# Kernel tuning notes

Measured on AMD Instinct MI355X. Metric: run time of the kernel, lower is better.

## Reference

```python
import jax, jax.numpy as jnp
import numpy as np

D_MODEL = 256
N_LAYERS = 4
D_STATE = 16
EXPAND = 2
D_CONV = 4
D_INNER = EXPAND * D_MODEL
DT_RANK = (D_MODEL + 15) // 16  # ceil(d_model/16) = 16
BATCH = 8
SEQ = 2048
EPS = 1e-5


def setup_inputs() -> dict:
    key = jax.random.key(0)
    ks = jax.random.split(key, 12)
    rn = lambda k, s, sc=0.02: jax.random.normal(k, s, dtype=jnp.float32) * sc
    A_log = jnp.log(jnp.broadcast_to(jnp.arange(1, D_STATE + 1, dtype=jnp.float32),
                                     (N_LAYERS, D_INNER, D_STATE)))
    return {
        "x": jax.random.normal(ks[0], (BATCH, SEQ, 2), dtype=jnp.float32),
        "w_in": rn(ks[1], (D_MODEL, 2), 0.5),
        "b_in": jnp.zeros((D_MODEL,), jnp.float32),
        "norm_w": jnp.ones((N_LAYERS, D_MODEL), jnp.float32),
        "in_proj_w": rn(ks[2], (N_LAYERS, 2 * D_INNER, D_MODEL)),
        "conv_w": rn(ks[3], (N_LAYERS, D_INNER, 1, D_CONV), 0.1),
        "conv_b": jnp.zeros((N_LAYERS, D_INNER), jnp.float32),
        "x_proj_w": rn(ks[4], (N_LAYERS, DT_RANK + 2 * D_STATE, D_INNER)),
        "dt_proj_w": rn(ks[5], (N_LAYERS, D_INNER, DT_RANK), 0.1),
        "dt_proj_b": rn(ks[6], (N_LAYERS, D_INNER), 0.1),
        "A_log": A_log,
        "D_skip": jnp.ones((N_LAYERS, D_INNER), jnp.float32),
        "out_proj_w": rn(ks[7], (N_LAYERS, D_MODEL, D_INNER)),
        "w_head": rn(ks[8], (1, D_MODEL), 0.1),
        "b_head": jnp.zeros((1,), jnp.float32),
    }


def _rmsnorm(x, w):
    return x * jax.lax.rsqrt(jnp.mean(x * x, axis=-1, keepdims=True) + EPS) * w


def _causal_dw_conv(x, w, b):
    # x: (B, L, C); w: (C, 1, K) depthwise; causal left-pad K-1
    xt = jnp.swapaxes(x, 1, 2)  # (B, C, L)
    y = jax.lax.conv_general_dilated(xt, w, (1,), [(D_CONV - 1, 0)],
                                     dimension_numbers=("NCH", "OIH", "NCH"),
                                     feature_group_count=D_INNER)
    return jnp.swapaxes(y + b[None, :, None], 1, 2)


def _selective_scan(u, delta, A, Bm, Cm, Dp):
    # u, delta: (B, L, E); A: (E, N); Bm, Cm: (B, L, N); Dp: (E,)
    dA = jnp.exp(delta[..., None] * A)                 # (B, L, E, N)
    dBu = (delta * u)[..., None] * Bm[:, :, None, :]   # (B, L, E, N)

    def step(h, t):
        dA_t, dBu_t = t
        h = dA_t * h + dBu_t
        return h, h

    h0 = jnp.zeros((u.shape[0], A.shape[0], A.shape[1]), u.dtype)
    _, hs = jax.lax.scan(step, h0, (jnp.swapaxes(dA, 0, 1), jnp.swapaxes(dBu, 0, 1)))
    y = jnp.einsum("lben,bln->ble", hs, Cm)            # (B, L, E)
    return y + u * Dp


def _mamba_block(x, in_w, cw, cb, xp_w, dtw, dtb, A_log, Dp, out_w):
    xz = x @ in_w.T                                    # (B, L, 2E)
    u, z = jnp.split(xz, 2, axis=-1)
    u = jax.nn.silu(_causal_dw_conv(u, cw, cb))
    dbc = u @ xp_w.T                                   # (B, L, dt_rank + 2N)
    delta = jax.nn.softplus(dbc[..., :DT_RANK] @ dtw.T + dtb)
    Bm = dbc[..., DT_RANK:DT_RANK + D_STATE]
    Cm = dbc[..., DT_RANK + D_STATE:]
    y = _selective_scan(u, delta, -jnp.exp(A_log), Bm, Cm, Dp)
    return (y * jax.nn.silu(z)) @ out_w.T


def reference(x, w_in, b_in, norm_w, in_proj_w, conv_w, conv_b, x_proj_w,
              dt_proj_w, dt_proj_b, A_log, D_skip, out_proj_w, w_head, b_head):
    h = x @ w_in.T + b_in                              # (B, L, d_model)
    for i in range(N_LAYERS):
        h = h + _mamba_block(_rmsnorm(h, norm_w[i]), in_proj_w[i], conv_w[i],
                             conv_b[i], x_proj_w[i], dt_proj_w[i], dt_proj_b[i],
                             A_log[i], D_skip[i], out_proj_w[i])
    return (h @ w_head.T + b_head)[..., 0]             # (B, L)
```

## Files before the change

kernel.cpp:

```cpp
#include <hip/hip_runtime.h>
#include <hip/hip_bf16.h>

#define BATCH 8
#define SEQ   2048
#define DM    256
#define DI    512
#define DS    16
#define DTR   16
#define NL    4
#define ROWS  (BATCH*SEQ)
#define NCH   32
#define CHL   64
#define NF    576

typedef __attribute__((ext_vector_type(8))) __bf16 bh8;
typedef __attribute__((ext_vector_type(4))) float f4;

#if __has_builtin(__builtin_amdgcn_exp2f)
#define EXP2(x) __builtin_amdgcn_exp2f(x)
#else
#define EXP2(x) exp2f(x)
#endif
#define LOG2E 1.4426950408889634f

__device__ __forceinline__ float bf2f(unsigned short u) {
    union { unsigned int i; float f; } v; v.i = ((unsigned int)u) << 16; return v.f;
}
__device__ __forceinline__ float4 us4f(ushort4 q) {
    return make_float4(bf2f(q.x), bf2f(q.y), bf2f(q.z), bf2f(q.w));
}
__device__ __forceinline__ float ldg1(const void* p, int i, int bf) {
    if (bf) return bf2f(((const unsigned short*)p)[i]);
    return ((const float*)p)[i];
}
__device__ __forceinline__ float4 ldg4(const void* p, int i, int bf) {
    if (bf) return us4f(*(const ushort4*)(((const unsigned short*)p) + i));
    return *(const float4*)(((const float*)p) + i);
}
__device__ __forceinline__ unsigned short f2bs(float f) {
    union { float f; unsigned u; } x; x.f = f;
    unsigned r = (x.u + 0x7fffu + ((x.u >> 16) & 1u)) >> 16;
    return (unsigned short)r;
}
__device__ __forceinline__ float fsilu(float x) {
    return x * __builtin_amdgcn_rcpf(1.0f + __expf(-x));
}
__device__ __forceinline__ float fsoftplus(float x) {
    return (x > 15.0f) ? x : __logf(1.0f + __expf(x));
}
__device__ __forceinline__ void pow16(float e1, float* pw) {
    float p2 = e1 * e1, p3 = p2 * e1, p4 = p2 * p2;
    float p5 = p4 * e1, p6 = p4 * p2, p7 = p4 * p3, p8 = p4 * p4;
    pw[0] = e1; pw[1] = p2; pw[2] = p3; pw[3] = p4;
    pw[4] = p5; pw[5] = p6; pw[6] = p7; pw[7] = p8;
    pw[8]  = p8 * e1; pw[9]  = p8 * p2; pw[10] = p8 * p3; pw[11] = p8 * p4;
    pw[12] = p8 * p5; pw[13] = p8 * p6; pw[14] = p8 * p7; pw[15] = p8 * p8;
}

typedef const __attribute__((address_space(1))) unsigned int* gas_t;
typedef __attribute__((address_space(3))) unsigned int* las_t;
__device__ __forceinline__ void gl16(const void* g, void* l) {
    __builtin_amdgcn_global_load_lds((gas_t)g, (las_t)l, 16, 0, 0);
}

__global__ void k_probe(const void* x, const void* A_log, int* flag) {
    int t = threadIdx.x;
    float v = bf2f(((const unsigned short*)x)[2 * t]);
    int bad = (fabsf(v) < 32.0f) ? 0 : 1;
    for (int o = 1; o < 64; o <<= 1) bad += __shfl_xor(bad, o);
    int bf = (bad > 8) ? 0 : 1;
    int nb = 0;
    for (int j = 0; j < 64; j++) {
        int e = ((j * 64 + t) * 17) & 32767;
        int n = e & 15;
        float a = ldg1(A_log, e, bf);
        float ea = __expf(a);
        if (fabsf(ea - (float)(n + 1)) > 0.02f * (float)(n + 1)) nb = 1;
    }
    for (int o = 1; o < 64; o <<= 1) nb += __shfl_xor(nb, o);
    if (t == 0) { flag[0] = bf; flag[1] = (nb == 0) ? 1 : 0; }
}

__global__ __launch_bounds__(256) void k_prep(const void* dtw, const void* xpw,
                                              unsigned short* Wc, const int* flag) {
    int bf = *flag;
    int blk = blockIdx.x;
    int l = blk / NF, r = blk % NF;
    int t = threadIdx.x;
    unsigned short* out = Wc + ((size_t)l * NF + r) * DI;
#pragma unroll
    for (int p = 0; p < 2; p++) {
        int k = t + p * 256;
        float v = 0.0f;
        if (r < 512) {
            const int db = l * DI * DTR + r * DTR;
            const int xb = l * 48 * DI;
#pragma unroll
            for (int j = 0; j < 16; j++)
                v = fmaf(ldg1(dtw, db + j, bf), ldg1(xpw, xb + j * DI + k, bf), v);
        } else if (r < 544) {
            v = ldg1(xpw, l * 48 * DI + (16 + r - 512) * DI + k, bf);
        }
        out[k] = f2bs(v);
    }
}

__global__ __launch_bounds__(256) void k_prepw(const void* ipw, const void* norm_w,
                                               unsigned short* Wip, const int* flag) {
    int bf = *flag;
    int blk = blockIdx.x;
    int l = blk >> 10, r = blk & 1023;
    int t = threadIdx.x;
    float v = ldg1(ipw, (l * 1024 + r) * 256 + t, bf) * ldg1(norm_w, l * 256 + t, bf);
    Wip[((size_t)l * 1024 + r) * 256 + t] = f2bs(v);
}

__global__ __launch_bounds__(256) void k_inproj(const void* x, const void* w_in, const void* b_in,
                                                unsigned short* h, float* rssq, const int* flag) {
    int bf = *flag;
    int row = blockIdx.x, e = threadIdx.x;
    float x0 = ldg1(x, row * 2 + 0, bf), x1 = ldg1(x, row * 2 + 1, bf);
    float w0 = ldg1(w_in, e * 2 + 0, bf), w1 = ldg1(w_in, e * 2 + 1, bf);
    float bb = ldg1(b_in, e, bf);
    unsigned short hb = f2bs(fmaf(x0, w0, fmaf(x1, w1, bb)));
    h[(size_t)row * DM + e] = hb;
    float hv = bf2f(hb);
    float ss = hv * hv;
#pragma unroll
    for (int o = 1; o < 64; o <<= 1) ss += __shfl_xor(ss, o);
    if ((e & 63) == 0) rssq[(size_t)row * 4 + (e >> 6)] = ss;
}

#define ASTR 72

__global__ __launch_bounds__(256, 4) void k_ipconv(const unsigned short* A, const unsigned short* W,
                                                   int w_off, unsigned short* xz, unsigned short* u,
                                                   const float* rssq, const void* cw, const void* cb,
                                                   int layer, const int* flag) {
    int bf = *flag;
    constexpr int K = DM;
    constexpr int TSTR = 136;
    __shared__ unsigned short SMEM[144 * TSTR];
    unsigned short* As  = SMEM;
    unsigned short* As2 = SMEM + 8192;
    unsigned short* Ws  = SMEM + 9216;

    int bm = blockIdx.x, bn = blockIdx.y;
    bool ublk = (bn < 4);
    int t = threadIdx.x;
    int w = t >> 6, lane = t & 63;
    int wm = w >> 1, wn = w & 1;
    int lr = lane & 15, quad = lane >> 4;
    int crow = lane >> 3;
    int ccol = ((lane & 7) ^ (lane >> 3)) * 8;

    f4 acc[4][4];
    f4 acc5[4];
#pragma unroll
    for (int i = 0; i < 4; i++) {
        acc5[i] = f4{0.f, 0.f, 0.f, 0.f};
#pragma unroll
        for (int j = 0; j < 4; j++) acc[i][j] = f4{0.f, 0.f, 0.f, 0.f};
    }

    for (int k0 = 0; k0 < K; k0 += 64) {
        __syncthreads();
#pragma unroll
        for (int i = 0; i < 4; i++) {
            int ci = w * 4 + i;
            int r = ci * 8 + crow;
            gl16(A + (size_t)(bm * 128 + r) * K + k0 + ccol, &As[ci * 512]);
        }
        if (ublk && w < 2) {
            int rg = bm * 128 - 16 + w * 8 + crow;
            if (rg < 0) rg = 0;
            gl16(A + (size_t)rg * K + k0 + ccol, &As2[w * 512]);
        }
#pragma unroll
        for (int i = 0; i < 4; i++) {
            int ci = w * 4 + i;
            int r = ci * 8 + crow;
            gl16(W + (size_t)w_off + (size_t)(bn * 128 + r) * K + k0 + ccol, &Ws[ci * 512]);
        }
        __syncthreads();
#pragma unroll
        for (int ks = 0; ks < 64; ks += 32) {
            int csw = (ks + quad * 8) ^ ((lr & 7) << 3);
            bh8 af[4];
#pragma unroll
            for (int i = 0; i < 4; i++)
                af[i] = *(const bh8*)&As[(wm * 64 + i * 16 + lr) * 64 + csw];
            bh8 wf[4];
#pragma unroll
            for (int j = 0; j < 4; j++)
                wf[j] = *(const bh8*)&Ws[(wn * 64 + j * 16 + lr) * 64 + csw];
#pragma unroll
            for (int i = 0; i < 4; i++)
#pragma unroll
                for (int j = 0; j < 4; j++)
                    acc[i][j] = __builtin_amdgcn_mfma_f32_16x16x32_bf16(af[i], wf[j], acc[i][j], 0, 0, 0);
            if (ublk && wm == 0) {
                bh8 a5 = *(const bh8*)&As2[lr * 64 + csw];
#pragma unroll
                for (int j = 0; j < 4; j++)
                    acc5[j] = __builtin_amdgcn_mfma_f32_16x16x32_bf16(a5, wf[j], acc5[j], 0, 0, 0);
            }
        }
    }
    __syncthreads();
    unsigned short* Tile = SMEM;
#pragma unroll
    for (int i = 0; i < 4; i++) {
        int rl = wm * 64 + i * 16 + quad * 4;
        float sc4[4];
#pragma unroll
        for (int r = 0; r < 4; r++) {
            float4 q4 = *(const float4*)&rssq[(size_t)(bm * 128 + rl + r) * 4];
            sc4[r] = rsqrtf((q4.x + q4.y + q4.z + q4.w) * (1.0f / (float)DM) + 1e-5f);
        }
#pragma unroll
        for (int j = 0; j < 4; j++) {
            int cl = wn * 64 + j * 16 + lr;
#pragma unroll
            for (int r = 0; r < 4; r++)
                Tile[(rl + r) * TSTR + cl] = f2bs(acc[i][j][r] * sc4[r]);
        }
    }
    if (ublk && wm == 0) {
#pragma unroll
        for (int r = 0; r < 4; r++) {
            int er = quad * 4 + r;
            int rg = bm * 128 - 16 + er;
            if (rg < 0) rg = 0;
            float4 q4 = *(const float4*)&rssq[(size_t)rg * 4];
            float sc = rsqrtf((q4.x + q4.y + q4.z + q4.w) * (1.0f / (float)DM) + 1e-5f);
#pragma unroll
            for (int j = 0; j < 4; j++) {
                int cl = wn * 64 + j * 16 + lr;
                Tile[(128 + er) * TSTR + cl] = f2bs(acc5[j][r] * sc);
            }
        }
    }
    __syncthreads();
    if (!ublk) {
#pragma unroll
        for (int i = 0; i < 8; i++) {
            int ch = t + i * 256;
            int r = ch >> 4, qc = (ch & 15) * 8;
            uint4 v = *(uint4*)&Tile[r * TSTR + qc];
            *(uint4*)&xz[(size_t)(bm * 128 + r) * 1024 + bn * 128 + qc] = v;
        }
    } else {
        int col4 = t & 31, rowg = t >> 5;
        int c0 = col4 * 4;
        int dg = bn * 128 + c0;
        float4 wv0 = ldg4(cw, (layer * DI + dg + 0) * 4, bf);
        float4 wv1 = ldg4(cw, (layer * DI + dg + 1) * 4, bf);
        float4 wv2 = ldg4(cw, (layer * DI + dg + 2) * 4, bf);
        float4 wv3 = ldg4(cw, (layer * DI + dg + 3) * 4, bf);
        float4 bb = ldg4(cb, layer * DI + dg, bf);
        bool bstart = ((bm & 15) == 0);
        int r0 = rowg * 16;
        auto ldrow = [&](int q) -> float4 {
            if (q < 0) {
                if (bstart) return make_float4(0.f, 0.f, 0.f, 0.f);
                return us4f(*(const ushort4*)&Tile[(144 + q) * TSTR + c0]);
            }
            return us4f(*(const ushort4*)&Tile[q * TSTR + c0]);
        };
        float4 xm3 = ldrow(r0 - 3), xm2 = ldrow(r0 - 2), xm1 = ldrow(r0 - 1);
        for (int rr = r0; rr < r0 + 16; rr++) {
            float4 x0 = us4f(*(const ushort4*)&Tile[rr * TSTR + c0]);
            float a0 = bb.x; a0 = fmaf(wv0.x, xm3.x, a0); a0 = fmaf(wv0.y, xm2.x, a0); a0 = fmaf(wv0.z, xm1.x, a0); a0 = fmaf(wv0.w, x0.x, a0);
            float a1 = bb.y; a1 = fmaf(wv1.x, xm3.y, a1); a1 = fmaf(wv1.y, xm2.y, a1); a1 = fmaf(wv1.z, xm1.y, a1); a1 = fmaf(wv1.w, x0.y, a1);
            float a2 = bb.z; a2 = fmaf(wv2.x, xm3.z, a2); a2 = fmaf(wv2.y, xm2.z, a2); a2 = fmaf(wv2.z, xm1.z, a2); a2 = fmaf(wv2.w, x0.z, a2);
            float a3 = bb.w; a3 = fmaf(wv3.x, xm3.w, a3); a3 = fmaf(wv3.y, xm2.w, a3); a3 = fmaf(wv3.z, xm1.w, a3); a3 = fmaf(wv3.w, x0.w, a3);
            ushort4 o = { f2bs(fsilu(a0)), f2bs(fsilu(a1)), f2bs(fsilu(a2)), f2bs(fsilu(a3)) };
            *(ushort4*)&u[(size_t)(bm * 128 + rr) * DI + dg] = o;
            xm3 = xm2; xm2 = xm1; xm1 = x0;
        }
    }
}

template <int BN, bool ADD, bool SCALE, bool RSUM, bool WINT>
__global__ __launch_bounds__(256, 4) void k_mfma(const unsigned short* A, const void* W, int w_off,
                                                 unsigned short* Cp, float* rssq,
                                                 int N, int K, const int* flag) {
    int bf = *flag;
    __shared__ unsigned short SMEM[(128 + BN) * ASTR];
    unsigned short* As = SMEM;
    unsigned short* Ws = SMEM + 128 * 64;
    constexpr int NT = BN / 32;
    constexpr int TSTR = BN + 8;

    int bm = blockIdx.x, bn = blockIdx.y;
    int t = threadIdx.x;
    int w = t >> 6, lane = t & 63;
    int wm = w >> 1, wn = w & 1;
    int lr = lane & 15, quad = lane >> 4;
    int crow = lane >> 3;
    int ccol = ((lane & 7) ^ (lane >> 3)) * 8;

    f4 acc[4][NT];
#pragma unroll
    for (int i = 0; i < 4; i++)
#pragma unroll
        for (int j = 0; j < NT; j++) acc[i][j] = f4{0.f, 0.f, 0.f, 0.f};

    for (int k0 = 0; k0 < K; k0 += 64) {
        __syncthreads();
#pragma unroll
        for (int i = 0; i < 4; i++) {
            int ci = w * 4 + i;
            int r = ci * 8 + crow;
            gl16(A + (size_t)(bm * 128 + r) * K + k0 + ccol, &As[ci * 512]);
        }
        if (WINT || bf) {
#pragma unroll
            for (int i = 0; i < BN / 32; i++) {
                int ci = w * (BN / 32) + i;
                int r = ci * 8 + crow;
                gl16((const unsigned short*)W + (size_t)w_off +
                         (size_t)(bn * BN + r) * K + k0 + ccol,
                     &Ws[ci * 512]);
            }
        } else {
#pragma unroll
            for (int i = 0; i < BN * 8 / 256; i++) {
                int ch = t + i * 256;
                int r = ch >> 3, kc = (ch & 7) * 8;
                size_t off = (size_t)w_off + (size_t)(bn * BN + r) * K + k0 + kc;
                const float* src = (const float*)W + off;
                float4 a0 = *(const float4*)src;
                float4 a1 = *(const float4*)(src + 4);
                ushort4 v0 = { f2bs(a0.x), f2bs(a0.y), f2bs(a0.z), f2bs(a0.w) };
                ushort4 v1 = { f2bs(a1.x), f2bs(a1.y), f2bs(a1.z), f2bs(a1.w) };
                unsigned short* dst = &Ws[r * 64 + (kc ^ ((r & 7) << 3))];
                *(ushort4*)dst = v0;
                *(ushort4*)(dst + 4) = v1;
            }
        }
        __syncthreads();
#pragma unroll
        for (int ks = 0; ks < 64; ks += 32) {
            int csw = (ks + quad * 8) ^ ((lr & 7) << 3);
            bh8 af[4];
#pragma unroll
            for (int i = 0; i < 4; i++)
                af[i] = *(const bh8*)&As[(wm * 64 + i * 16 + lr) * 64 + csw];
            bh8 wf[NT];
#pragma unroll
            for (int j = 0; j < NT; j++)
                wf[j] = *(const bh8*)&Ws[(wn * (BN / 2) + j * 16 + lr) * 64 + csw];
#pragma unroll
            for (int i = 0; i < 4; i++)
#pragma unroll
                for (int j = 0; j < NT; j++)
                    acc[i][j] = __builtin_amdgcn_mfma_f32_16x16x32_bf16(af[i], wf[j], acc[i][j], 0, 0, 0);
        }
    }
    __syncthreads();
    unsigned short* Tile = SMEM;
#pragma unroll
    for (int i = 0; i < 4; i++) {
        int rl = wm * 64 + i * 16 + quad * 4;
        float sc4[4];
        if (SCALE) {
#pragma unroll
            for (int r = 0; r < 4; r++) {
                float4 q4 = *(const float4*)&rssq[(size_t)(bm * 128 + rl + r) * 4];
                sc4[r] = rsqrtf((q4.x + q4.y + q4.z + q4.w) * (1.0f / (float)DM) + 1e-5f);
            }
        }
#pragma unroll
        for (int j = 0; j < NT; j++) {
            int cl = wn * (BN / 2) + j * 16 + lr;
#pragma unroll
            for (int r = 0; r < 4; r++) {
                float vv = acc[i][j][r];
                if (SCALE) vv *= sc4[r];
                Tile[(rl + r) * TSTR + cl] = f2bs(vv);
            }
        }
    }
    __syncthreads();
    constexpr int CPT = 128 * BN / 8 / 256;
#pragma unroll
    for (int i = 0; i < CPT; i++) {
        int ch = t + i * 256;
        int r = ch / (BN / 8), qc = (ch % (BN / 8)) * 8;
        uint4 v = *(uint4*)&Tile[r * TSTR + qc];
        size_t gidx = (size_t)(bm * 128 + r) * N + bn * BN + qc;
        if (ADD) {
            uint4 c = *(uint4*)&Cp[gidx];
            unsigned short* vp = (unsigned short*)&v;
            unsigned short* cp2 = (unsigned short*)&c;
            uint4 ov;
            unsigned short* op = (unsigned short*)&ov;
            float ssq = 0.0f;
#pragma unroll
            for (int e = 0; e < 8; e++) {
                op[e] = f2bs(bf2f(vp[e]) + bf2f(cp2[e]));
                if (RSUM) { float hv = bf2f(op[e]); ssq = fmaf(hv, hv, ssq); }
            }
            *(uint4*)&Cp[gidx] = ov;
            if (RSUM) {
#pragma unroll
                for (int o2 = 1; o2 < 8; o2 <<= 1) ssq += __shfl_xor(ssq, o2);
                if ((lane & 7) == 0) rssq[(size_t)(bm * 128 + r) * 4 + bn] = ssq;
            }
        } else {
            *(uint4*)&Cp[gidx] = v;
        }
    }
}

__global__ __launch_bounds__(256, 4) void k_fused(const unsigned short* A, const unsigned short* Wc,
                                                  int w_off, unsigned short* delta, float* BC,
                                                  const void* dtb, int layer, const int* flag) {
    int bf = *flag;
    __shared__ unsigned short SMEM[(128 + 64) * ASTR];
    unsigned short* As = SMEM;
    unsigned short* Ws = SMEM + 128 * 64;
    constexpr int TSTR = 72;

    int bm = blockIdx.x, bn = blockIdx.y;
    int t = threadIdx.x;
    int w = t >> 6, lane = t & 63;
    int wm = w >> 1, wn = w & 1;
    int lr = lane & 15, quad = lane >> 4;
    int crow = lane >> 3;
    int ccol = ((lane & 7) ^ (lane >> 3)) * 8;

    f4 acc[4][2];
#pragma unroll
    for (int i = 0; i < 4; i++)
#pragma unroll
        for (int j = 0; j < 2; j++) acc[i][j] = f4{0.f, 0.f, 0.f, 0.f};

    for (int k0 = 0; k0 < DI; k0 += 64) {
        __syncthreads();
#pragma unroll
        for (int i = 0; i < 4; i++) {
            int ci = w * 4 + i;
            int r = ci * 8 + crow;
            gl16(A + (size_t)(bm * 128 + r) * DI + k0 + ccol, &As[ci * 512]);
        }
#pragma unroll
        for (int i = 0; i < 2; i++) {
            int ci = w * 2 + i;
            int r = ci * 8 + crow;
            gl16(Wc + (size_t)w_off + (size_t)(bn * 64 + r) * DI + k0 + ccol, &Ws[ci * 512]);
        }
        __syncthreads();
#pragma unroll
        for (int ks = 0; ks < 64; ks += 32) {
            int csw = (ks + quad * 8) ^ ((lr & 7) << 3);
            bh8 af[4];
#pragma unroll
            for (int i = 0; i < 4; i++)
                af[i] = *(const bh8*)&As[(wm * 64 + i * 16 + lr) * 64 + csw];
            bh8 wf[2];
#pragma unroll
            for (int j = 0; j < 2; j++)
                wf[j] = *(const bh8*)&Ws[(wn * 32 + j * 16 + lr) * 64 + csw];
#pragma unroll
            for (int i = 0; i < 4; i++)
#pragma unroll
                for (int j = 0; j < 2; j++)
                    acc[i][j] = __builtin_amdgcn_mfma_f32_16x16x32_bf16(af[i], wf[j], acc[i][j], 0, 0, 0);
        }
    }
    if (bn < 8) {
        __syncthreads();
        unsigned short* Tile = SMEM;
#pragma unroll
        for (int i = 0; i < 4; i++) {
            int rl = wm * 64 + i * 16 + quad * 4;
#pragma unroll
            for (int j = 0; j < 2; j++) {
                int cl = wn * 32 + j * 16 + lr;
                float bb = ldg1(dtb, layer * DI + bn * 64 + cl, bf);
#pragma unroll
                for (int r = 0; r < 4; r++)
                    Tile[(rl + r) * TSTR + cl] = f2bs(fsoftplus(acc[i][j][r] + bb));
            }
        }
        __syncthreads();
#pragma unroll
        for (int i = 0; i < 4; i++) {
            int ch = t + i * 256;
            int r = ch >> 3, qc = (ch & 7) * 8;
            uint4 v = *(uint4*)&Tile[r * TSTR + qc];
            *(uint4*)&delta[(size_t)(bm * 128 + r) * DI + bn * 64 + qc] = v;
        }
    } else {
#pragma unroll
        for (int i = 0; i < 4; i++) {
            int row0 = bm * 128 + wm * 64 + i * 16 + quad * 4;
#pragma unroll
            for (int j = 0; j < 2; j++) {
                int col = bn * 64 + wn * 32 + j * 16 + lr;
                if (col < 544) {
#pragma unroll
                    for (int r = 0; r < 4; r++)
                        BC[(size_t)(row0 + r) * 32 + (col - 512)] = acc[i][j][r];
                }
            }
        }
    }
}

__global__ __launch_bounds__(256) void k_scan1(const unsigned short* delta, const unsigned short* u,
                                               const float* BC, const void* A_log, float* Sb, float* E,
                                               int layer, const int* flag) {
    int bf = flag[0], sA = flag[1];
    int x = blockIdx.x;
    int dg = x & 1, c = (x >> 1) & (NCH - 1), b = x >> 6;
    int tid = threadIdx.x;
    int d = dg * 256 + tid;
    int t0 = c * CHL;

    __shared__ float sB[CHL][16];
    {
        int r = tid >> 2, q = tid & 3;
        *(float4*)&sB[r][q * 4] =
            *(const float4*)(BC + ((size_t)b * SEQ + t0 + r) * 32 + q * 4);
    }

    float A2[16];
#pragma unroll
    for (int n4 = 0; n4 < 4; n4++) {
        float4 a4 = ldg4(A_log, (layer * DI + d) * DS + n4 * 4, bf);
        A2[n4 * 4 + 0] = -__expf(a4.x) * LOG2E;
        A2[n4 * 4 + 1] = -__expf(a4.y) * LOG2E;
        A2[n4 * 4 + 2] = -__expf(a4.z) * LOG2E;
        A2[n4 * 4 + 3] = -__expf(a4.w) * LOG2E;
    }
    float h[16];
#pragma unroll
    for (int n = 0; n < 16; n++) h[n] = 0.0f;
    float S = 0.0f;

    const unsigned short* dp = delta + ((size_t)b * SEQ + t0) * DI + d;
    const unsigned short* up = u + ((size_t)b * SEQ + t0) * DI + d;

    float dl0[4], uu0[4];
#pragma unroll
    for (int j = 0; j < 4; j++) { dl0[j] = bf2f(dp[j * DI]); uu0[j] = bf2f(up[j * DI]); }
    __syncthreads();

    for (int s = 0; s < CHL / 4; s++) {
        int sn = (s + 1 < CHL / 4) ? (s + 1) : s;
        float dl1[4], uu1[4];
#pragma unroll
        for (int j = 0; j < 4; j++) {
            dl1[j] = bf2f(dp[(sn * 4 + j) * DI]);
            uu1[j] = bf2f(up[(sn * 4 + j) * DI]);
        }
#pragma unroll
        for (int j = 0; j < 4; j++) {
            int t = s * 4 + j;
            float dlt = dl0[j], uu = uu0[j];
            float du = dlt * uu;
            S += dlt;
            if (sA) {
                float pw[16];
                pow16(EXP2(-dlt * LOG2E), pw);
#pragma unroll
                for (int n4 = 0; n4 < 4; n4++) {
                    float4 Bv = *(const float4*)&sB[t][n4 * 4];
                    int n = n4 * 4;
                    h[n + 0] = fmaf(pw[n + 0], h[n + 0], du * Bv.x);
                    h[n + 1] = fmaf(pw[n + 1], h[n + 1], du * Bv.y);
                    h[n + 2] = fmaf(pw[n + 2], h[n + 2], du * Bv.z);
                    h[n + 3] = fmaf(pw[n + 3], h[n + 3], du * Bv.w);
                }
            } else {
#pragma unroll
                for (int n4 = 0; n4 < 4; n4++) {
                    float4 Bv = *(const float4*)&sB[t][n4 * 4];
                    int n = n4 * 4;
                    float a0 = EXP2(dlt * A2[n + 0]); h[n + 0] = fmaf(a0, h[n + 0], du * Bv.x);
                    float a1 = EXP2(dlt * A2[n + 1]); h[n + 1] = fmaf(a1, h[n + 1], du * Bv.y);
                    float a2 = EXP2(dlt * A2[n + 2]); h[n + 2] = fmaf(a2, h[n + 2], du * Bv.z);
                    float a3 = EXP2(dlt * A2[n + 3]); h[n + 3] = fmaf(a3, h[n + 3], du * Bv.w);
                }
            }
        }
#pragma unroll
        for (int j = 0; j < 4; j++) { dl0[j] = dl1[j]; uu0[j] = uu1[j]; }
    }
    Sb[((size_t)b * NCH + c) * DI + d] = S;
    float* Ed = E + (((size_t)b * NCH + c) * DI + d) * DS;
#pragma unroll
    for (int n4 = 0; n4 < 4; n4++)
        *(float4*)(Ed + n4 * 4) = make_float4(h[n4 * 4], h[n4 * 4 + 1], h[n4 * 4 + 2], h[n4 * 4 + 3]);
}

__global__ __launch_bounds__(256) void k_scan2(const unsigned short* delta, const unsigned short* u,
                                               const float* BC, const void* A_log, const void* D_skip,
                                               const unsigned short* xz, const float* Sb, const float* E,
                                               unsigned short* g, int layer, const int* flag) {
    int bf = flag[0], sA = flag[1];
    int x = blockIdx.x;
    int dg = x & 1, c = (x >> 1) & (NCH - 1), b = x >> 6;
    int tid = threadIdx.x;
    int d = dg * 256 + tid;
    int t0 = c * CHL;

    __shared__ float sBC[CHL][32];
#pragma unroll
    for (int k2 = 0; k2 < 2; k2++) {
        int fi = k2 * 256 + tid;
        int r = fi >> 3, q = fi & 7;
        *(float4*)&sBC[r][q * 4] =
            *(const float4*)(BC + ((size_t)b * SEQ + t0 + r) * 32 + q * 4);
    }

    float A2[16];
#pragma unroll
    for (int n4 = 0; n4 < 4; n4++) {
        float4 a4 = ldg4(A_log, (layer * DI + d) * DS + n4 * 4, bf);
        A2[n4 * 4 + 0] = -__expf(a4.x) * LOG2E;
        A2[n4 * 4 + 1] = -__expf(a4.y) * LOG2E;
        A2[n4 * 4 + 2] = -__expf(a4.z) * LOG2E;
        A2[n4 * 4 + 3] = -__expf(a4.w) * LOG2E;
    }
    float Dp = ldg1(D_skip, layer * DI + d, bf);

    float h[16];
#pragma unroll
    for (int n = 0; n < 16; n++) h[n] = 0.0f;
    for (int cc = 0; cc < c; cc++) {
        float S = Sb[((size_t)b * NCH + cc) * DI + d];
        const float* Ep = E + (((size_t)b * NCH + cc) * DI + d) * DS;
        if (sA) {
            float pw[16];
            pow16(EXP2(-S * LOG2E), pw);
#pragma unroll
            for (int n4 = 0; n4 < 4; n4++) {
                float4 e4 = *(const float4*)(Ep + n4 * 4);
                int n = n4 * 4;
                h[n + 0] = fmaf(pw[n + 0], h[n + 0], e4.x);
                h[n + 1] = fmaf(pw[n + 1], h[n + 1], e4.y);
                h[n + 2] = fmaf(pw[n + 2], h[n + 2], e4.z);
                h[n + 3] = fmaf(pw[n + 3], h[n + 3], e4.w);
            }
        } else {
#pragma unroll
            for (int n4 = 0; n4 < 4; n4++) {
                float4 e4 = *(const float4*)(Ep + n4 * 4);
                int n = n4 * 4;
                h[n + 0] = fmaf(EXP2(A2[n + 0] * S), h[n + 0], e4.x);
                h[n + 1] = fmaf(EXP2(A2[n + 1] * S), h[n + 1], e4.y);
                h[n + 2] = fmaf(EXP2(A2[n + 2] * S), h[n + 2], e4.z);
                h[n + 3] = fmaf(EXP2(A2[n + 3] * S), h[n + 3], e4.w);
            }
        }
    }

    const unsigned short* dp = delta + ((size_t)b * SEQ + t0) * DI + d;
    const unsigned short* up = u + ((size_t)b * SEQ + t0) * DI + d;
    const unsigned short* zp = xz + ((size_t)b * SEQ + t0) * (2 * DI) + DI + d;
    unsigned short* gp = g + ((size_t)b * SEQ + t0) * DI + d;

    float dl0[4], uu0[4], zz0[4];
#pragma unroll
    for (int j = 0; j < 4; j++) {
        dl0[j] = bf2f(dp[j * DI]); uu0[j] = bf2f(up[j * DI]); zz0[j] = bf2f(zp[j * (2 * DI)]);
    }
    __syncthreads();

    for (int s = 0; s < CHL / 4; s++) {
        int sn = (s + 1 < CHL / 4) ? (s + 1) : s;
        float dl1[4], uu1[4], zz1[4];
#pragma unroll
        for (int j = 0; j < 4; j++) {
            dl1[j] = bf2f(dp[(sn * 4 + j) * DI]);
            uu1[j] = bf2f(up[(sn * 4 + j) * DI]);
            zz1[j] = bf2f(zp[(sn * 4 + j) * (2 * DI)]);
        }
#pragma unroll
        for (int j = 0; j < 4; j++) {
            int t = s * 4 + j;
            float dlt = dl0[j], uu = uu0[j], zz = zz0[j];
            float du = dlt * uu;
            float y = 0.0f;
            if (sA) {
                float pw[16];
                pow16(EXP2(-dlt * LOG2E), pw);
#pragma unroll
                for (int n4 = 0; n4 < 4; n4++) {
                    float4 Bv = *(const float4*)&sBC[t][n4 * 4];
                    float4 Cv = *(const float4*)&sBC[t][16 + n4 * 4];
                    int n = n4 * 4;
                    h[n + 0] = fmaf(pw[n + 0], h[n + 0], du * Bv.x); y = fmaf(Cv.x, h[n + 0], y);
                    h[n + 1] = fmaf(pw[n + 1], h[n + 1], du * Bv.y); y = fmaf(Cv.y, h[n + 1], y);
                    h[n + 2] = fmaf(pw[n + 2], h[n + 2], du * Bv.z); y = fmaf(Cv.z, h[n + 2], y);
                    h[n + 3] = fmaf(pw[n + 3], h[n + 3], du * Bv.w); y = fmaf(Cv.w, h[n + 3], y);
                }
            } else {
#pragma unroll
                for (int n4 = 0; n4 < 4; n4++) {
                    float4 Bv = *(const float4*)&sBC[t][n4 * 4];
                    float4 Cv = *(const float4*)&sBC[t][16 + n4 * 4];
                    int n = n4 * 4;
                    float a0 = EXP2(dlt * A2[n + 0]); h[n + 0] = fmaf(a0, h[n + 0], du * Bv.x); y = fmaf(Cv.x, h[n + 0], y);
                    float a1 = EXP2(dlt * A2[n + 1]); h[n + 1] = fmaf(a1, h[n + 1], du * Bv.y); y = fmaf(Cv.y, h[n + 1], y);
                    float a2 = EXP2(dlt * A2[n + 2]); h[n + 2] = fmaf(a2, h[n + 2], du * Bv.z); y = fmaf(Cv.z, h[n + 2], y);
                    float a3 = EXP2(dlt * A2[n + 3]); h[n + 3] = fmaf(a3, h[n + 3], du * Bv.w); y = fmaf(Cv.w, h[n + 3], y);
                }
            }
            float yt = fmaf(uu, Dp, y);
            gp[(size_t)t * DI] = f2bs(yt * fsilu(zz));
        }
#pragma unroll
        for (int j = 0; j < 4; j++) { dl0[j] = dl1[j]; uu0[j] = uu1[j]; zz0[j] = zz1[j]; }
    }
}

__global__ __launch_bounds__(256) void k_head(const unsigned short* h, const void* w_head,
                                              const void* b_head, void* out, const int* flag) {
    int bf = *flag;
    int wv = threadIdx.x >> 6, ln = threadIdx.x & 63;
    int row = blockIdx.x * 4 + wv;
    float4 v = us4f(*(const ushort4*)(h + (size_t)row * DM + ln * 4));
    float4 w = ldg4(w_head, ln * 4, bf);
    float s = v.x * w.x + v.y * w.y + v.z * w.z + v.w * w.w;
    for (int o = 1; o < 64; o <<= 1) s += __shfl_xor(s, o);
    if (ln == 0) {
        s += ldg1(b_head, 0, bf);
        if (bf) ((__hip_bfloat16*)out)[row] = __float2bfloat16(s);
        else    ((float*)out)[row] = s;
    }
}

extern "C" void kernel_launch(void* const* d_in, const int* in_sizes, int n_in,
                              void* d_out, int out_size, void* d_ws, size_t ws_size,
                              hipStream_t stream) {
    (void)in_sizes; (void)n_in; (void)out_size; (void)ws_size;
    const void* x      = d_in[0];
    const void* w_in   = d_in[1];
    const void* b_in   = d_in[2];
    const void* norm_w = d_in[3];
    const void* ipw    = d_in[4];
    const void* cw     = d_in[5];
    const void* cb     = d_in[6];
    const void* xpw    = d_in[7];
    const void* dtw    = d_in[8];
    const void* dtb    = d_in[9];
    const void* A_log  = d_in[10];
    const void* D_skip = d_in[11];
    const void* opw    = d_in[12];
    const void* w_head = d_in[13];
    const void* b_head = d_in[14];

    float* ws    = (float*)d_ws;
    unsigned short* h     = (unsigned short*)ws;
    float*          rssq  = ws + 4194304;
    float*          Sb    = ws + 4194304;
    float*          E     = ws + 4718592;
    unsigned short* xz    = (unsigned short*)(ws + 8388608);
    unsigned short* u     = (unsigned short*)(ws + 25165824);
    float*          BC    = ws + 33554432;
    unsigned short* delta = (unsigned short*)(ws + 34340864);
    unsigned short* Wcomb = (unsigned short*)(ws + 38535168);
    unsigned short* Wipc  = (unsigned short*)(ws + 39124992);
    int*            flag  = (int*)(ws + 42729472);

    k_probe<<<1, 64, 0, stream>>>(x, A_log, flag);
    k_prep<<<NL * NF, 256, 0, stream>>>(dtw, xpw, Wcomb, flag);
    k_prepw<<<NL * 1024, 256, 0, stream>>>(ipw, norm_w, Wipc, flag);
    k_inproj<<<ROWS, 256, 0, stream>>>(x, w_in, b_in, h, rssq, flag);

    for (int layer = 0; layer < NL; layer++) {
        k_ipconv<<<dim3(ROWS / 128, 8), 256, 0, stream>>>(
            h, Wipc, layer * 2 * DI * DM, xz, u, rssq, cw, cb, layer, flag);
        k_fused<<<dim3(ROWS / 128, NF / 64), 256, 0, stream>>>(
            u, Wcomb, layer * NF * DI, delta, BC, dtb, layer, flag);
        k_scan1<<<BATCH * NCH * 2, 256, 0, stream>>>(delta, u, BC, A_log, Sb, E, layer, flag);
        k_scan2<<<BATCH * NCH * 2, 256, 0, stream>>>(delta, u, BC, A_log, D_skip, xz, Sb, E,
                                                     u , layer, flag);
        k_mfma<64, true, false, true, false><<<dim3(ROWS / 128, DM / 64), 256, 0, stream>>>(
            u, opw, layer * DM * DI, h, rssq, DM, DI, flag);
    }

    k_head<<<ROWS / 4, 256, 0, stream>>>(h, w_head, b_head, d_out, flag);
}
```

Before: 604.2 us.

## Add stitch kernel to sequentially combine chunk states instead of per-block prefix recompute

```diff
diff --git a/kernel.cpp b/kernel.cpp
--- a/kernel.cpp
+++ b/kernel.cpp
@@ -598,9 +598,27 @@
         *(float4*)(Ed + n4 * 4) = make_float4(h[n4 * 4], h[n4 * 4 + 1], h[n4 * 4 + 2], h[n4 * 4 + 3]);
 }
 
+__global__ __launch_bounds__(256) void k_stitch(const float* Sb, const void* A_log, float* E,
+                                                int layer, const int* flag) {
+    int bf = flag[0];
+    int g = blockIdx.x * 256 + threadIdx.x;
+    int b = g >> 13, r = g & 8191;
+    int d = r >> 4;
+    float A2a = -__expf(ldg1(A_log, (layer * DI + d) * DS + (r & 15), bf)) * LOG2E;
+    size_t ebase = (size_t)b * NCH * (DI * DS) + r;
+    float H = 0.0f;
+    for (int c = 0; c < NCH; c++) {
+        float p = EXP2(A2a * Sb[((size_t)b * NCH + c) * DI + d]);
+        size_t idx = ebase + (size_t)c * (DI * DS);
+        float e = E[idx];
+        E[idx] = H;
+        H = fmaf(p, H, e);
+    }
+}
+
 __global__ __launch_bounds__(256) void k_scan2(const unsigned short* delta, const unsigned short* u,
                                                const float* BC, const void* A_log, const void* D_skip,
-                                               const unsigned short* xz, const float* Sb, const float* E,
+                                               const unsigned short* xz, const float* E,
                                                unsigned short* g, int layer, const int* flag) {
     int bf = flag[0], sA = flag[1];
     int x = blockIdx.x;
@@ -630,34 +648,11 @@
     float Dp = ldg1(D_skip, layer * DI + d, bf);
 
     float h[16];
-#pragma unroll
-    for (int n = 0; n < 16; n++) h[n] = 0.0f;
-    for (int cc = 0; cc < c; cc++) {
-        float S = Sb[((size_t)b * NCH + cc) * DI + d];
-        const float* Ep = E + (((size_t)b * NCH + cc) * DI + d) * DS;
-        if (sA) {
-            float pw[16];
-            pow16(EXP2(-S * LOG2E), pw);
-#pragma unroll
-            for (int n4 = 0; n4 < 4; n4++) {
-                float4 e4 = *(const float4*)(Ep + n4 * 4);
-                int n = n4 * 4;
-                h[n + 0] = fmaf(pw[n + 0], h[n + 0], e4.x);
-                h[n + 1] = fmaf(pw[n + 1], h[n + 1], e4.y);
-                h[n + 2] = fmaf(pw[n + 2], h[n + 2], e4.z);
-                h[n + 3] = fmaf(pw[n + 3], h[n + 3], e4.w);
-            }
-        } else {
-#pragma unroll
-            for (int n4 = 0; n4 < 4; n4++) {
-                float4 e4 = *(const float4*)(Ep + n4 * 4);
-                int n = n4 * 4;
-                h[n + 0] = fmaf(EXP2(A2[n + 0] * S), h[n + 0], e4.x);
-                h[n + 1] = fmaf(EXP2(A2[n + 1] * S), h[n + 1], e4.y);
-                h[n + 2] = fmaf(EXP2(A2[n + 2] * S), h[n + 2], e4.z);
-                h[n + 3] = fmaf(EXP2(A2[n + 3] * S), h[n + 3], e4.w);
-            }
-        }
+    const float* E0 = E + (((size_t)b * NCH + c) * DI + d) * DS;
+#pragma unroll
+    for (int n4 = 0; n4 < 4; n4++) {
+        float4 h4 = *(const float4*)(E0 + n4 * 4);
+        h[n4 * 4 + 0] = h4.x; h[n4 * 4 + 1] = h4.y; h[n4 * 4 + 2] = h4.z; h[n4 * 4 + 3] = h4.w;
     }
 
     const unsigned short* dp = delta + ((size_t)b * SEQ + t0) * DI + d;
@@ -780,7 +775,8 @@
         k_fused<<<dim3(ROWS / 128, NF / 64), 256, 0, stream>>>(
             u, Wcomb, layer * NF * DI, delta, BC, dtb, layer, flag);
         k_scan1<<<BATCH * NCH * 2, 256, 0, stream>>>(delta, u, BC, A_log, Sb, E, layer, flag);
-        k_scan2<<<BATCH * NCH * 2, 256, 0, stream>>>(delta, u, BC, A_log, D_skip, xz, Sb, E,
+        k_stitch<<<BATCH * DI * DS / 256, 256, 0, stream>>>(Sb, A_log, E, layer, flag);
+        k_scan2<<<BATCH * NCH * 2, 256, 0, stream>>>(delta, u, BC, A_log, D_skip, xz, E,
                                                      u , layer, flag);
         k_mfma<64, true, false, true, false><<<dim3(ROWS / 128, DM / 64), 256, 0, stream>>>(
             u, opw, layer * DM * DI, h, rssq, DM, DI, flag);
```

Result: faster. 582.3 us (-3.6%).
